# Performance work log

Hardware: AMD Instinct MI355X
Metric: run time of the kernel (lower is better)

Reference implementation:

```python
import jax, jax.numpy as jnp
import numpy as np

N_NODES = 50000


def _glorot(key, fan_in, fan_out):
    limit = float(np.sqrt(6.0 / (fan_in + fan_out)))
    return jax.random.uniform(key, (fan_in, fan_out), jnp.float32, -limit, limit)


def setup_inputs() -> dict:
    key = jax.random.key(0)
    k_x, k_src, k_dst, k1, k2, k3 = jax.random.split(key, 6)
    x = jax.random.normal(k_x, (N_NODES, 128), dtype=jnp.float32)
    src = jax.random.randint(k_src, (800000,), 0, N_NODES)
    dst = jax.random.randint(k_dst, (800000,), 0, N_NODES)
    edge_index = jnp.stack([src, dst]).astype(jnp.int64)  # [2, E]
    W1 = _glorot(k1, 128, 96)
    W2 = _glorot(k2, 96, 96)
    W3 = _glorot(k3, 96, 40)
    b1 = jnp.zeros((96,), jnp.float32)
    b2 = jnp.zeros((96,), jnp.float32)
    b3 = jnp.zeros((40,), jnp.float32)
    return {"x": x, "W1": W1, "b1": b1, "W2": W2, "b2": b2,
            "W3": W3, "b3": b3, "edge_index": edge_index}


def _aggregate(x, src, dst):
    # sparse adj SpMM with 'add' reduce: out[dst] += x[src]
    return jax.ops.segment_sum(x[src], dst, num_segments=N_NODES)


def reference(x, W1, b1, W2, b2, W3, b3, edge_index):
    src, dst = edge_index[0], edge_index[1]
    # layer 1: aggregate -> linear -> relu (dropout identity in eval)
    h = jax.nn.relu(_aggregate(x, src, dst) @ W1 + b1)
    # layer 2
    h = jax.nn.relu(_aggregate(h, src, dst) @ W2 + b2)
    # layer 3 + log_softmax
    logits = _aggregate(h, src, dst) @ W3 + b3
    return jax.nn.log_softmax(logits, axis=-1)
```

## Files before the change

### kernel.cpp

```cpp
#include <hip/hip_runtime.h>
#include <math.h>

typedef __attribute__((ext_vector_type(8))) short bf16x8;
typedef __attribute__((ext_vector_type(4))) float f32x4;

__device__ __forceinline__ unsigned short f2bf(float f) {
  unsigned u = __float_as_uint(f);
  u += 0x7fffu + ((u >> 16) & 1u);
  return (unsigned short)(u >> 16);
}
__device__ __forceinline__ float bflo(unsigned u) { return __uint_as_float(u << 16); }
__device__ __forceinline__ float bfhi(unsigned u) { return __uint_as_float(u & 0xffff0000u); }


constexpr int CB = 64;

__global__ __launch_bounds__(256) void count_pack_gemm1(
    const int* __restrict__ dst, int* __restrict__ partial, int E,
    const float* __restrict__ W1, const float* __restrict__ W2, const float* __restrict__ W3,
    unsigned short* __restrict__ Wp2, unsigned short* __restrict__ Wp3,
    const float* __restrict__ x, unsigned short* __restrict__ Tb, int N) {
  int tid = threadIdx.x;
  if (blockIdx.x < CB) {
    __shared__ int bkt[256];
    bkt[tid] = 0;
    __syncthreads();
    int E4 = E >> 2;
    const int4* d4 = (const int4*)dst;
    for (int i = blockIdx.x * 256 + tid; i < E4; i += CB * 256) {
      int4 d = d4[i];
      atomicAdd(&bkt[d.x >> 8], 1);
      atomicAdd(&bkt[d.y >> 8], 1);
      atomicAdd(&bkt[d.z >> 8], 1);
      atomicAdd(&bkt[d.w >> 8], 1);
    }
    if (blockIdx.x == 0 && tid < (E & 3)) atomicAdd(&bkt[dst[E4 * 4 + tid] >> 8], 1);
    __syncthreads();
    partial[blockIdx.x * 256 + tid] = bkt[tid];
    return;
  }
  if (blockIdx.x < CB + 7) {
    int gid = (blockIdx.x - CB) * 256 + tid;
    const float* W;
    unsigned short* Wp;
    int t, NCTT, M, MV;
    if (gid < 1152) {
      W = W2; Wp = Wp2; t = gid; NCTT = 6; M = 96; MV = 96;
    } else if (gid < 1728) {
      W = W3; Wp = Wp3; t = gid - 1152; NCTT = 3; M = 40; MV = 40;
    } else {
      return;
    }
    int lane = t & 63;
    int frag = t >> 6;
    int s = frag / NCTT;
    int ct = frag - s * NCTT;
    int colv = ct * 16 + (lane & 15);
    int k0 = s * 32 + (lane >> 4) * 8;
    union { unsigned short s[8]; uint4 u; } pk;
#pragma unroll
    for (int j = 0; j < 8; ++j) {
      float v = (colv < MV) ? W[(k0 + j) * M + colv] : 0.f;
      pk.s[j] = f2bf(v);
    }
    ((uint4*)Wp)[t] = pk.u;
    return;
  }
  int bgx = blockIdx.x - CB - 7;
  int wid = tid >> 6;
  int lane = tid & 63;
  int rt = bgx * 4 + wid;
  if (rt * 16 >= N) return;
  int quad = lane >> 4;
  int lm = lane & 15;
  bf16x8 bfrag[4][6];
#pragma unroll
  for (int s = 0; s < 4; ++s)
#pragma unroll
    for (int c = 0; c < 6; ++c) {
      union { unsigned short s[8]; bf16x8 v; } bu;
      int k0 = s * 32 + quad * 8;
      int colv = c * 16 + lm;
#pragma unroll
      for (int j = 0; j < 8; ++j) bu.s[j] = f2bf(W1[(k0 + j) * 96 + colv]);
      bfrag[s][c] = bu.v;
    }
  f32x4 acc[6];
#pragma unroll
  for (int c = 0; c < 6; ++c) acc[c] = (f32x4){0.f, 0.f, 0.f, 0.f};
  int row = rt * 16 + lm;
  if (row >= N) row = N - 1;
#pragma unroll
  for (int s = 0; s < 4; ++s) {
    int k0 = s * 32 + quad * 8;
    const float* Af = x + (size_t)row * 128 + k0;
    float4 x0 = *(const float4*)(Af);
    float4 x1 = *(const float4*)(Af + 4);
    union { unsigned short s[8]; bf16x8 v; } au;
    au.s[0] = f2bf(x0.x); au.s[1] = f2bf(x0.y); au.s[2] = f2bf(x0.z); au.s[3] = f2bf(x0.w);
    au.s[4] = f2bf(x1.x); au.s[5] = f2bf(x1.y); au.s[6] = f2bf(x1.z); au.s[7] = f2bf(x1.w);
#pragma unroll
    for (int c = 0; c < 6; ++c)
      acc[c] = __builtin_amdgcn_mfma_f32_16x16x32_bf16(au.v, bfrag[s][c], acc[c], 0, 0, 0);
  }
#pragma unroll
  for (int c = 0; c < 6; ++c) {
    int colv = c * 16 + lm;
#pragma unroll
    for (int r = 0; r < 4; ++r) {
      int orow = rt * 16 + quad * 4 + r;
      if (orow < N) Tb[(size_t)orow * 96 + colv] = f2bf(acc[c][r]);
    }
  }
}

__global__ __launch_bounds__(256) void scan_kernel(const int* __restrict__ partial,
                                                   int* __restrict__ gstart,
                                                   int* __restrict__ gcur,
                                                   int* __restrict__ row_ptr,
                                                   int NB, int N, int E) {
  int tid = threadIdx.x;
  int s = 0;
#pragma unroll 8
  for (int i = 0; i < CB; ++i) s += partial[i * 256 + tid];
  __shared__ int sm[256];
  sm[tid] = s;
  __syncthreads();
  for (int off = 1; off < 256; off <<= 1) {
    int u = (tid >= off) ? sm[tid - off] : 0;
    __syncthreads();
    sm[tid] += u;
    __syncthreads();
  }
  int excl = sm[tid] - s;
  if (tid < NB) { gstart[tid] = excl; gcur[tid] = excl; }
  if (tid == NB - 1) gstart[NB] = sm[tid];
  if (tid == 0) row_ptr[N] = E;
}

__global__ __launch_bounds__(256) void bin_edges(const int* __restrict__ src,
                                                 const int* __restrict__ dst,
                                                 int* __restrict__ gcur,
                                                 int* __restrict__ packed, int E, int NB) {
  __shared__ int lcnt[256];
  __shared__ int gbase[256];
  int tid = threadIdx.x;
  lcnt[tid] = 0;
  __syncthreads();
  int idx = blockIdx.x * 256 + tid;
  int E4 = E >> 2;
  int sv[4], dv[4], lv[4];
  int cnt = 0;
  if (idx < E4) {
    int4 s4 = ((const int4*)src)[idx];
    int4 d4 = ((const int4*)dst)[idx];
    sv[0] = s4.x; sv[1] = s4.y; sv[2] = s4.z; sv[3] = s4.w;
    dv[0] = d4.x; dv[1] = d4.y; dv[2] = d4.z; dv[3] = d4.w;
    cnt = 4;
  } else if (idx == E4 && (E & 3)) {
    int tl = E & 3;
    for (int i = 0; i < tl; ++i) { sv[i] = src[E4 * 4 + i]; dv[i] = dst[E4 * 4 + i]; }
    cnt = tl;
  }
  for (int i = 0; i < cnt; ++i) lv[i] = atomicAdd(&lcnt[dv[i] >> 8], 1);
  __syncthreads();
  if (tid < NB) gbase[tid] = atomicAdd(&gcur[tid], lcnt[tid]);
  __syncthreads();
  for (int i = 0; i < cnt; ++i) {
    int b = dv[i] >> 8;
    packed[gbase[b] + lv[i]] = ((dv[i] & 255) << 16) | (sv[i] & 0xffff);
  }
}

__global__ __launch_bounds__(256) void build_local_csr(const int* __restrict__ packed,
                                                       const int* __restrict__ gstart,
                                                       int* __restrict__ row_ptr,
                                                       int* __restrict__ col, int N) {
  __shared__ int cnt[256];
  __shared__ int sm[256];
  int b = blockIdx.x, tid = threadIdx.x;
  int gs = gstart[b], ge = gstart[b + 1];
  int me = ge - gs;
  int node0 = b << 8;
  int RL = N - node0;
  if (RL > 256) RL = 256;
  cnt[tid] = 0;
  __syncthreads();
  for (int i = tid; i < me; i += 256) atomicAdd(&cnt[packed[gs + i] >> 16], 1);
  __syncthreads();
  int v = cnt[tid];
  sm[tid] = v;
  __syncthreads();
  for (int off = 1; off < 256; off <<= 1) {
    int u = (tid >= off) ? sm[tid - off] : 0;
    __syncthreads();
    sm[tid] += u;
    __syncthreads();
  }
  int excl = gs + sm[tid] - v;
  __syncthreads();
  cnt[tid] = excl;
  if (tid < RL) row_ptr[node0 + tid] = excl;
  __syncthreads();
  for (int i = tid; i < me; i += 256) {
    int pk = packed[gs + i];
    int p = atomicAdd(&cnt[pk >> 16], 1);
    col[p] = pk & 0xffff;
  }
}


template <int NCT, int MOUT, int MVALID>
__global__ __launch_bounds__(256) void fused_agg_gemm(const unsigned short* __restrict__ tin,
                                                      const int* __restrict__ row_ptr,
                                                      const int* __restrict__ col,
                                                      const float* __restrict__ bias,
                                                      const unsigned short* __restrict__ Wp,
                                                      unsigned short* __restrict__ outp, int N) {
  constexpr int LST = 104;
  constexpr int CAP = 2048;
  __shared__ unsigned short sH[64 * LST];
  __shared__ int scol[CAP];
  __shared__ int srp[65];
  int tid = threadIdx.x;
  int node0 = blockIdx.x * 64;
  int nloc = N - node0;
  if (nloc > 64) nloc = 64;
  if (tid <= nloc) srp[tid] = row_ptr[node0 + tid];
  __syncthreads();
  int gs = srp[0];
  int me = srp[nloc] - gs;
  for (int i = tid; i < me && i < CAP; i += 256) scol[i] = col[gs + i];
  __syncthreads();

#pragma unroll
  for (int it = 0; it < 3; ++it) {
    int u = tid + it * 256;
    int nl = u / 12;
    int c = u - nl * 12;
    if (nl < nloc) {
      int beg = srp[nl] - gs;
      int end = srp[nl + 1] - gs;
      const unsigned short* tc = tin + 8 * c;
      float a0 = 0.f, a1 = 0.f, a2 = 0.f, a3 = 0.f, a4 = 0.f, a5 = 0.f, a6 = 0.f, a7 = 0.f;
      int e = beg;
      for (; e + 1 < end; e += 2) {
        int s0 = (e < CAP) ? scol[e] : col[gs + e];
        int s1 = (e + 1 < CAP) ? scol[e + 1] : col[gs + e + 1];
        uint4 u4 = *(const uint4*)(tc + (size_t)s0 * 96);
        uint4 w4 = *(const uint4*)(tc + (size_t)s1 * 96);
        a0 += bflo(u4.x); a1 += bfhi(u4.x);
        a2 += bflo(u4.y); a3 += bfhi(u4.y);
        a4 += bflo(u4.z); a5 += bfhi(u4.z);
        a6 += bflo(u4.w); a7 += bfhi(u4.w);
        a0 += bflo(w4.x); a1 += bfhi(w4.x);
        a2 += bflo(w4.y); a3 += bfhi(w4.y);
        a4 += bflo(w4.z); a5 += bfhi(w4.z);
        a6 += bflo(w4.w); a7 += bfhi(w4.w);
      }
      if (e < end) {
        int s0 = (e < CAP) ? scol[e] : col[gs + e];
        uint4 u4 = *(const uint4*)(tc + (size_t)s0 * 96);
        a0 += bflo(u4.x); a1 += bfhi(u4.x);
        a2 += bflo(u4.y); a3 += bfhi(u4.y);
        a4 += bflo(u4.z); a5 += bfhi(u4.z);
        a6 += bflo(u4.w); a7 += bfhi(u4.w);
      }
      const float* b = bias + 8 * c;
      union { unsigned short s[8]; uint4 u; } pk;
      pk.s[0] = f2bf(fmaxf(a0 + b[0], 0.f));
      pk.s[1] = f2bf(fmaxf(a1 + b[1], 0.f));
      pk.s[2] = f2bf(fmaxf(a2 + b[2], 0.f));
      pk.s[3] = f2bf(fmaxf(a3 + b[3], 0.f));
      pk.s[4] = f2bf(fmaxf(a4 + b[4], 0.f));
      pk.s[5] = f2bf(fmaxf(a5 + b[5], 0.f));
      pk.s[6] = f2bf(fmaxf(a6 + b[6], 0.f));
      pk.s[7] = f2bf(fmaxf(a7 + b[7], 0.f));
      *(uint4*)&sH[nl * LST + c * 8] = pk.u;
    }
  }
  __syncthreads();

  int wid = tid >> 6;
  int lane = tid & 63;
  int rt16 = wid * 16;
  if (node0 + rt16 >= N) return;
  int quad = lane >> 4;
  int lm = lane & 15;
  union BU { uint4 u; bf16x8 v; };
  bf16x8 bfrag[3][NCT];
  const uint4* wp4 = (const uint4*)Wp;
#pragma unroll
  for (int s = 0; s < 3; ++s)
#pragma unroll
    for (int c = 0; c < NCT; ++c) {
      BU bu;
      bu.u = wp4[(s * NCT + c) * 64 + lane];
      bfrag[s][c] = bu.v;
    }
  f32x4 acc[NCT];
#pragma unroll
  for (int c = 0; c < NCT; ++c) acc[c] = (f32x4){0.f, 0.f, 0.f, 0.f};
#pragma unroll
  for (int s = 0; s < 3; ++s) {
    BU au;
    au.u = *(const uint4*)&sH[(rt16 + lm) * LST + s * 32 + quad * 8];
#pragma unroll
    for (int c = 0; c < NCT; ++c)
      acc[c] = __builtin_amdgcn_mfma_f32_16x16x32_bf16(au.v, bfrag[s][c], acc[c], 0, 0, 0);
  }
#pragma unroll
  for (int c = 0; c < NCT; ++c) {
    int colv = c * 16 + lm;
    if (colv >= MVALID) continue;
#pragma unroll
    for (int r = 0; r < 4; ++r) {
      int orow = node0 + rt16 + quad * 4 + r;
      if (orow < N) outp[(size_t)orow * MOUT + colv] = f2bf(acc[c][r]);
    }
  }
}

__global__ __launch_bounds__(256) void agg_lsm_bf16(const unsigned short* __restrict__ t,
                                                    const int* __restrict__ row_ptr,
                                                    const int* __restrict__ col,
                                                    const float* __restrict__ bias,
                                                    float* __restrict__ out, int N) {
  constexpr int CAPL = 1024;
  __shared__ int scol[CAPL];
  __shared__ int srp[17];
  int tid = threadIdx.x;
  int node0 = blockIdx.x * 16;
  int nloc = N - node0;
  if (nloc > 16) nloc = 16;
  if (tid <= nloc) srp[tid] = row_ptr[node0 + tid];
  __syncthreads();
  int gs = srp[0];
  int me = srp[nloc] - gs;
  for (int i = tid; i < me && i < CAPL; i += 256) scol[i] = col[gs + i];
  __syncthreads();

  int nl = tid >> 4;
  int c = tid & 15;
  bool act = (c < 10) && (nl < nloc);
  int ceff = (c < 10) ? c : 0;
  const unsigned short* tc = t + 4 * ceff;
  float v0 = 0.f, v1 = 0.f, v2 = 0.f, v3 = 0.f;
  if (act) {
    int beg = srp[nl] - gs;
    int end = srp[nl + 1] - gs;
    int e = beg;
    for (; e + 1 < end; e += 2) {
      int s0 = (e < CAPL) ? scol[e] : col[gs + e];
      int s1 = (e + 1 < CAPL) ? scol[e + 1] : col[gs + e + 1];
      uint2 u = *(const uint2*)(tc + (size_t)s0 * 40);
      uint2 w = *(const uint2*)(tc + (size_t)s1 * 40);
      v0 += bflo(u.x); v1 += bfhi(u.x);
      v2 += bflo(u.y); v3 += bfhi(u.y);
      v0 += bflo(w.x); v1 += bfhi(w.x);
      v2 += bflo(w.y); v3 += bfhi(w.y);
    }
    if (e < end) {
      int s0 = (e < CAPL) ? scol[e] : col[gs + e];
      uint2 u = *(const uint2*)(tc + (size_t)s0 * 40);
      v0 += bflo(u.x); v1 += bfhi(u.x);
      v2 += bflo(u.y); v3 += bfhi(u.y);
    }
  }
  const float* bb = bias + 4 * ceff;
  v0 += bb[0]; v1 += bb[1]; v2 += bb[2]; v3 += bb[3];
  float m = act ? fmaxf(fmaxf(v0, v1), fmaxf(v2, v3)) : -__builtin_inff();
#pragma unroll
  for (int off = 8; off; off >>= 1) m = fmaxf(m, __shfl_xor(m, off, 64));
  float ex = act ? (__expf(v0 - m) + __expf(v1 - m) + __expf(v2 - m) + __expf(v3 - m)) : 0.f;
#pragma unroll
  for (int off = 8; off; off >>= 1) ex += __shfl_xor(ex, off, 64);
  if (act) {
    int node = node0 + nl;
    float l = m + __logf(ex);
    float* o = out + (size_t)node * 40 + 4 * c;
    o[0] = v0 - l; o[1] = v1 - l; o[2] = v2 - l; o[3] = v3 - l;
  }
}


extern "C" void kernel_launch(void* const* d_in, const int* in_sizes, int n_in,
                              void* d_out, int out_size, void* d_ws, size_t ws_size,
                              hipStream_t stream) {
  const float* x  = (const float*)d_in[0];
  const float* W1 = (const float*)d_in[1];
  const float* b1 = (const float*)d_in[2];
  const float* W2 = (const float*)d_in[3];
  const float* b2 = (const float*)d_in[4];
  const float* W3 = (const float*)d_in[5];
  const float* b3 = (const float*)d_in[6];
  const int* edge = (const int*)d_in[7];

  int N = in_sizes[0] / 128;
  int E = in_sizes[7] / 2;
  const int* srcp = edge;
  const int* dstp = edge + E;

  char* p = (char*)d_ws;
  auto alloc = [&](size_t bytes) {
    char* r = p;
    p += (bytes + 255) & ~size_t(255);
    return r;
  };
  int NB = (N + 255) >> 8;
  int* partial = (int*)alloc((size_t)CB * 256 * 4);
  int* gstart  = (int*)alloc((size_t)(NB + 1) * 4);
  int* gcur    = (int*)alloc((size_t)NB * 4);
  int* row_ptr = (int*)alloc((size_t)(N + 1) * 4);
  int* packed  = (int*)alloc((size_t)E * 4);
  int* col     = (int*)alloc((size_t)E * 4);
  unsigned short* Wp2 = (unsigned short*)alloc(1152 * 8 * 2);
  unsigned short* Wp3 = (unsigned short*)alloc(576 * 8 * 2);
  unsigned short* Tb  = (unsigned short*)alloc((size_t)N * 96 * 2);
  unsigned short* T2b = (unsigned short*)alloc((size_t)N * 96 * 2);
  unsigned short* T3b = (unsigned short*)alloc((size_t)N * 40 * 2);

  int E4 = E >> 2;
  int nbin = (E4 + ((E & 3) ? 1 : 0) + 255) / 256;
  int GB = ((N + 15) / 16 + 3) / 4;
  int FB = (N + 63) / 64;

  count_pack_gemm1<<<CB + 7 + GB, 256, 0, stream>>>(dstp, partial, E, W1, W2, W3,
                                                    Wp2, Wp3, x, Tb, N);
  scan_kernel<<<1, 256, 0, stream>>>(partial, gstart, gcur, row_ptr, NB, N, E);
  bin_edges<<<nbin, 256, 0, stream>>>(srcp, dstp, gcur, packed, E, NB);
  build_local_csr<<<NB, 256, 0, stream>>>(packed, gstart, row_ptr, col, N);
  fused_agg_gemm<6, 96, 96><<<FB, 256, 0, stream>>>(Tb, row_ptr, col, b1, Wp2, T2b, N);
  fused_agg_gemm<3, 40, 40><<<FB, 256, 0, stream>>>(T2b, row_ptr, col, b2, Wp3, T3b, N);
  agg_lsm_bf16<<<(N + 15) / 16, 256, 0, stream>>>(T3b, row_ptr, col, b3, (float*)d_out, N);
}
```

Measured before the change: 209.8 us.

## Move layer-1 GEMM into binning kernel, prepack W1, unroll gathers by four

W1 is now pre-packed to bf16 MFMA fragments in the count/pack kernel. The layer-1 x@W1 GEMM moves from the counting kernel into the edge-binning kernel, so it overlaps with binning, and it reads the packed W1 instead of converting W1 in every wave. The neighbour-gather loops in the aggregation kernels are unrolled from two to four loads in flight. fused_agg_gemm gets a min-waves occupancy hint and loads B fragments inside the MFMA loop instead of keeping them all in registers. These changes target per-wave conversion cost, register pressure and gather latency, at the risk of a longer critical path through bin_gemm1 and extra global loads of weight fragments.

```diff
diff --git a/kernel.cpp b/kernel.cpp
--- a/kernel.cpp
+++ b/kernel.cpp
@@ -15,11 +15,14 @@
 
 constexpr int CB = 64;
 
-__global__ __launch_bounds__(256) void count_pack_gemm1(
-    const int* __restrict__ dst, int* __restrict__ partial, int E,
-    const float* __restrict__ W1, const float* __restrict__ W2, const float* __restrict__ W3,
-    unsigned short* __restrict__ Wp2, unsigned short* __restrict__ Wp3,
-    const float* __restrict__ x, unsigned short* __restrict__ Tb, int N) {
+__global__ __launch_bounds__(256) void count_pack(const int* __restrict__ dst,
+                                                  int* __restrict__ partial, int E,
+                                                  const float* __restrict__ W1,
+                                                  const float* __restrict__ W2,
+                                                  const float* __restrict__ W3,
+                                                  unsigned short* __restrict__ Wp1,
+                                                  unsigned short* __restrict__ Wp2,
+                                                  unsigned short* __restrict__ Wp3) {
   int tid = threadIdx.x;
   if (blockIdx.x < CB) {
     __shared__ int bkt[256];
@@ -39,79 +42,32 @@
     partial[blockIdx.x * 256 + tid] = bkt[tid];
     return;
   }
-  if (blockIdx.x < CB + 7) {
-    int gid = (blockIdx.x - CB) * 256 + tid;
-    const float* W;
-    unsigned short* Wp;
-    int t, NCTT, M, MV;
-    if (gid < 1152) {
-      W = W2; Wp = Wp2; t = gid; NCTT = 6; M = 96; MV = 96;
-    } else if (gid < 1728) {
-      W = W3; Wp = Wp3; t = gid - 1152; NCTT = 3; M = 40; MV = 40;
-    } else {
-      return;
-    }
-    int lane = t & 63;
-    int frag = t >> 6;
-    int s = frag / NCTT;
-    int ct = frag - s * NCTT;
-    int colv = ct * 16 + (lane & 15);
-    int k0 = s * 32 + (lane >> 4) * 8;
-    union { unsigned short s[8]; uint4 u; } pk;
-#pragma unroll
-    for (int j = 0; j < 8; ++j) {
-      float v = (colv < MV) ? W[(k0 + j) * M + colv] : 0.f;
-      pk.s[j] = f2bf(v);
-    }
-    ((uint4*)Wp)[t] = pk.u;
+  int gid = (blockIdx.x - CB) * 256 + tid;
+  const float* W;
+  unsigned short* Wp;
+  int t, NCTT, M, MV;
+  if (gid < 1536) {
+    W = W1; Wp = Wp1; t = gid; NCTT = 6; M = 96; MV = 96;
+  } else if (gid < 2688) {
+    W = W2; Wp = Wp2; t = gid - 1536; NCTT = 6; M = 96; MV = 96;
+  } else if (gid < 3264) {
+    W = W3; Wp = Wp3; t = gid - 2688; NCTT = 3; M = 40; MV = 40;
+  } else {
     return;
   }
-  int bgx = blockIdx.x - CB - 7;
-  int wid = tid >> 6;
-  int lane = tid & 63;
-  int rt = bgx * 4 + wid;
-  if (rt * 16 >= N) return;
-  int quad = lane >> 4;
-  int lm = lane & 15;
-  bf16x8 bfrag[4][6];
-#pragma unroll
-  for (int s = 0; s < 4; ++s)
-#pragma unroll
-    for (int c = 0; c < 6; ++c) {
-      union { unsigned short s[8]; bf16x8 v; } bu;
-      int k0 = s * 32 + quad * 8;
-      int colv = c * 16 + lm;
-#pragma unroll
-      for (int j = 0; j < 8; ++j) bu.s[j] = f2bf(W1[(k0 + j) * 96 + colv]);
-      bfrag[s][c] = bu.v;
-    }
-  f32x4 acc[6];
-#pragma unroll
-  for (int c = 0; c < 6; ++c) acc[c] = (f32x4){0.f, 0.f, 0.f, 0.f};
-  int row = rt * 16 + lm;
-  if (row >= N) row = N - 1;
-#pragma unroll
-  for (int s = 0; s < 4; ++s) {
-    int k0 = s * 32 + quad * 8;
-    const float* Af = x + (size_t)row * 128 + k0;
-    float4 x0 = *(const float4*)(Af);
-    float4 x1 = *(const float4*)(Af + 4);
-    union { unsigned short s[8]; bf16x8 v; } au;
-    au.s[0] = f2bf(x0.x); au.s[1] = f2bf(x0.y); au.s[2] = f2bf(x0.z); au.s[3] = f2bf(x0.w);
-    au.s[4] = f2bf(x1.x); au.s[5] = f2bf(x1.y); au.s[6] = f2bf(x1.z); au.s[7] = f2bf(x1.w);
-#pragma unroll
-    for (int c = 0; c < 6; ++c)
-      acc[c] = __builtin_amdgcn_mfma_f32_16x16x32_bf16(au.v, bfrag[s][c], acc[c], 0, 0, 0);
-  }
-#pragma unroll
-  for (int c = 0; c < 6; ++c) {
-    int colv = c * 16 + lm;
-#pragma unroll
-    for (int r = 0; r < 4; ++r) {
-      int orow = rt * 16 + quad * 4 + r;
-      if (orow < N) Tb[(size_t)orow * 96 + colv] = f2bf(acc[c][r]);
-    }
-  }
+  int lane = t & 63;
+  int frag = t >> 6;
+  int s = frag / NCTT;
+  int ct = frag - s * NCTT;
+  int colv = ct * 16 + (lane & 15);
+  int k0 = s * 32 + (lane >> 4) * 8;
+  union { unsigned short s[8]; uint4 u; } pk;
+#pragma unroll
+  for (int j = 0; j < 8; ++j) {
+    float v = (colv < MV) ? W[(k0 + j) * M + colv] : 0.f;
+    pk.s[j] = f2bf(v);
+  }
+  ((uint4*)Wp)[t] = pk.u;
 }
 
 __global__ __launch_bounds__(256) void scan_kernel(const int* __restrict__ partial,
@@ -138,37 +94,82 @@
   if (tid == 0) row_ptr[N] = E;
 }
 
-__global__ __launch_bounds__(256) void bin_edges(const int* __restrict__ src,
+__global__ __launch_bounds__(256) void bin_gemm1(const int* __restrict__ src,
                                                  const int* __restrict__ dst,
                                                  int* __restrict__ gcur,
-                                                 int* __restrict__ packed, int E, int NB) {
-  __shared__ int lcnt[256];
-  __shared__ int gbase[256];
+                                                 int* __restrict__ packed, int E, int NB,
+                                                 int NBIN, const float* __restrict__ x,
+                                                 const unsigned short* __restrict__ Wp1,
+                                                 unsigned short* __restrict__ Tb, int N) {
   int tid = threadIdx.x;
-  lcnt[tid] = 0;
-  __syncthreads();
-  int idx = blockIdx.x * 256 + tid;
-  int E4 = E >> 2;
-  int sv[4], dv[4], lv[4];
-  int cnt = 0;
-  if (idx < E4) {
-    int4 s4 = ((const int4*)src)[idx];
-    int4 d4 = ((const int4*)dst)[idx];
-    sv[0] = s4.x; sv[1] = s4.y; sv[2] = s4.z; sv[3] = s4.w;
-    dv[0] = d4.x; dv[1] = d4.y; dv[2] = d4.z; dv[3] = d4.w;
-    cnt = 4;
-  } else if (idx == E4 && (E & 3)) {
-    int tl = E & 3;
-    for (int i = 0; i < tl; ++i) { sv[i] = src[E4 * 4 + i]; dv[i] = dst[E4 * 4 + i]; }
-    cnt = tl;
-  }
-  for (int i = 0; i < cnt; ++i) lv[i] = atomicAdd(&lcnt[dv[i] >> 8], 1);
-  __syncthreads();
-  if (tid < NB) gbase[tid] = atomicAdd(&gcur[tid], lcnt[tid]);
-  __syncthreads();
-  for (int i = 0; i < cnt; ++i) {
-    int b = dv[i] >> 8;
-    packed[gbase[b] + lv[i]] = ((dv[i] & 255) << 16) | (sv[i] & 0xffff);
+  if (blockIdx.x < NBIN) {
+    __shared__ int lcnt[256];
+    __shared__ int gbase[256];
+    lcnt[tid] = 0;
+    __syncthreads();
+    int idx = blockIdx.x * 256 + tid;
+    int E4 = E >> 2;
+    int sv[4], dv[4], lv[4];
+    int cnt = 0;
+    if (idx < E4) {
+      int4 s4 = ((const int4*)src)[idx];
+      int4 d4 = ((const int4*)dst)[idx];
+      sv[0] = s4.x; sv[1] = s4.y; sv[2] = s4.z; sv[3] = s4.w;
+      dv[0] = d4.x; dv[1] = d4.y; dv[2] = d4.z; dv[3] = d4.w;
+      cnt = 4;
+    } else if (idx == E4 && (E & 3)) {
+      int tl = E & 3;
+      for (int i = 0; i < tl; ++i) { sv[i] = src[E4 * 4 + i]; dv[i] = dst[E4 * 4 + i]; }
+      cnt = tl;
+    }
+    for (int i = 0; i < cnt; ++i) lv[i] = atomicAdd(&lcnt[dv[i] >> 8], 1);
+    __syncthreads();
+    if (tid < NB) gbase[tid] = atomicAdd(&gcur[tid], lcnt[tid]);
+    __syncthreads();
+    for (int i = 0; i < cnt; ++i) {
+      int b = dv[i] >> 8;
+      packed[gbase[b] + lv[i]] = ((dv[i] & 255) << 16) | (sv[i] & 0xffff);
+    }
+    return;
+  }
+  int bx = blockIdx.x - NBIN;
+  int wid = tid >> 6;
+  int lane = tid & 63;
+  int rt = bx * 4 + wid;
+  if (rt * 16 >= N) return;
+  int quad = lane >> 4;
+  int lm = lane & 15;
+  union BU { uint4 u; bf16x8 v; };
+  f32x4 acc[6];
+#pragma unroll
+  for (int c = 0; c < 6; ++c) acc[c] = (f32x4){0.f, 0.f, 0.f, 0.f};
+  int row = rt * 16 + lm;
+  if (row >= N) row = N - 1;
+  const uint4* wp4 = (const uint4*)Wp1;
+#pragma unroll
+  for (int s = 0; s < 4; ++s) {
+    int k0 = s * 32 + quad * 8;
+    const float* Af = x + (size_t)row * 128 + k0;
+    float4 x0 = *(const float4*)(Af);
+    float4 x1 = *(const float4*)(Af + 4);
+    union { unsigned short s[8]; bf16x8 v; } au;
+    au.s[0] = f2bf(x0.x); au.s[1] = f2bf(x0.y); au.s[2] = f2bf(x0.z); au.s[3] = f2bf(x0.w);
+    au.s[4] = f2bf(x1.x); au.s[5] = f2bf(x1.y); au.s[6] = f2bf(x1.z); au.s[7] = f2bf(x1.w);
+#pragma unroll
+    for (int c = 0; c < 6; ++c) {
+      BU bu;
+      bu.u = wp4[(s * 6 + c) * 64 + lane];
+      acc[c] = __builtin_amdgcn_mfma_f32_16x16x32_bf16(au.v, bu.v, acc[c], 0, 0, 0);
+    }
+  }
+#pragma unroll
+  for (int c = 0; c < 6; ++c) {
+    int colv = c * 16 + lm;
+#pragma unroll
+    for (int r = 0; r < 4; ++r) {
+      int orow = rt * 16 + quad * 4 + r;
+      if (orow < N) Tb[(size_t)orow * 96 + colv] = f2bf(acc[c][r]);
+    }
   }
 }
 
@@ -211,12 +212,10 @@
 
 
 template <int NCT, int MOUT, int MVALID>
-__global__ __launch_bounds__(256) void fused_agg_gemm(const unsigned short* __restrict__ tin,
-                                                      const int* __restrict__ row_ptr,
-                                                      const int* __restrict__ col,
-                                                      const float* __restrict__ bias,
-                                                      const unsigned short* __restrict__ Wp,
-                                                      unsigned short* __restrict__ outp, int N) {
+__global__ __launch_bounds__(256, 6) void fused_agg_gemm(
+    const unsigned short* __restrict__ tin, const int* __restrict__ row_ptr,
+    const int* __restrict__ col, const float* __restrict__ bias,
+    const unsigned short* __restrict__ Wp, unsigned short* __restrict__ outp, int N) {
   constexpr int LST = 104;
   constexpr int CAP = 2048;
   __shared__ unsigned short sH[64 * LST];
@@ -244,27 +243,29 @@
       const unsigned short* tc = tin + 8 * c;
       float a0 = 0.f, a1 = 0.f, a2 = 0.f, a3 = 0.f, a4 = 0.f, a5 = 0.f, a6 = 0.f, a7 = 0.f;
       int e = beg;
-      for (; e + 1 < end; e += 2) {
+      for (; e + 3 < end; e += 4) {
         int s0 = (e < CAP) ? scol[e] : col[gs + e];
         int s1 = (e + 1 < CAP) ? scol[e + 1] : col[gs + e + 1];
-        uint4 u4 = *(const uint4*)(tc + (size_t)s0 * 96);
-        uint4 w4 = *(const uint4*)(tc + (size_t)s1 * 96);
-        a0 += bflo(u4.x); a1 += bfhi(u4.x);
-        a2 += bflo(u4.y); a3 += bfhi(u4.y);
-        a4 += bflo(u4.z); a5 += bfhi(u4.z);
-        a6 += bflo(u4.w); a7 += bfhi(u4.w);
-        a0 += bflo(w4.x); a1 += bfhi(w4.x);
-        a2 += bflo(w4.y); a3 += bfhi(w4.y);
-        a4 += bflo(w4.z); a5 += bfhi(w4.z);
-        a6 += bflo(w4.w); a7 += bfhi(w4.w);
+        int s2 = (e + 2 < CAP) ? scol[e + 2] : col[gs + e + 2];
+        int s3 = (e + 3 < CAP) ? scol[e + 3] : col[gs + e + 3];
+        uint4 u0 = *(const uint4*)(tc + (size_t)s0 * 96);
+        uint4 u1 = *(const uint4*)(tc + (size_t)s1 * 96);
+        uint4 u2 = *(const uint4*)(tc + (size_t)s2 * 96);
+        uint4 u3 = *(const uint4*)(tc + (size_t)s3 * 96);
+        a0 += bflo(u0.x); a1 += bfhi(u0.x); a2 += bflo(u0.y); a3 += bfhi(u0.y);
+        a4 += bflo(u0.z); a5 += bfhi(u0.z); a6 += bflo(u0.w); a7 += bfhi(u0.w);
+        a0 += bflo(u1.x); a1 += bfhi(u1.x); a2 += bflo(u1.y); a3 += bfhi(u1.y);
+        a4 += bflo(u1.z); a5 += bfhi(u1.z); a6 += bflo(u1.w); a7 += bfhi(u1.w);
+        a0 += bflo(u2.x); a1 += bfhi(u2.x); a2 += bflo(u2.y); a3 += bfhi(u2.y);
+        a4 += bflo(u2.z); a5 += bfhi(u2.z); a6 += bflo(u2.w); a7 += bfhi(u2.w);
+        a0 += bflo(u3.x); a1 += bfhi(u3.x); a2 += bflo(u3.y); a3 += bfhi(u3.y);
+        a4 += bflo(u3.z); a5 += bfhi(u3.z); a6 += bflo(u3.w); a7 += bfhi(u3.w);
       }
-      if (e < end) {
+      for (; e < end; ++e) {
         int s0 = (e < CAP) ? scol[e] : col[gs + e];
         uint4 u4 = *(const uint4*)(tc + (size_t)s0 * 96);
-        a0 += bflo(u4.x); a1 += bfhi(u4.x);
-        a2 += bflo(u4.y); a3 += bfhi(u4.y);
-        a4 += bflo(u4.z); a5 += bfhi(u4.z);
-        a6 += bflo(u4.w); a7 += bfhi(u4.w);
+        a0 += bflo(u4.x); a1 += bfhi(u4.x); a2 += bflo(u4.y); a3 += bfhi(u4.y);
+        a4 += bflo(u4.z); a5 += bfhi(u4.z); a6 += bflo(u4.w); a7 += bfhi(u4.w);
       }
       const float* b = bias + 8 * c;
       union { unsigned short s[8]; uint4 u; } pk;
@@ -288,26 +289,20 @@
   int quad = lane >> 4;
   int lm = lane & 15;
   union BU { uint4 u; bf16x8 v; };
-  bf16x8 bfrag[3][NCT];
+  f32x4 acc[NCT];
+#pragma unroll
+  for (int c = 0; c < NCT; ++c) acc[c] = (f32x4){0.f, 0.f, 0.f, 0.f};
   const uint4* wp4 = (const uint4*)Wp;
 #pragma unroll
-  for (int s = 0; s < 3; ++s)
+  for (int s = 0; s < 3; ++s) {
+    BU au;
+    au.u = *(const uint4*)&sH[(rt16 + lm) * LST + s * 32 + quad * 8];
 #pragma unroll
     for (int c = 0; c < NCT; ++c) {
       BU bu;
       bu.u = wp4[(s * NCT + c) * 64 + lane];
-      bfrag[s][c] = bu.v;
-    }
-  f32x4 acc[NCT];
-#pragma unroll
-  for (int c = 0; c < NCT; ++c) acc[c] = (f32x4){0.f, 0.f, 0.f, 0.f};
-#pragma unroll
-  for (int s = 0; s < 3; ++s) {
-    BU au;
-    au.u = *(const uint4*)&sH[(rt16 + lm) * LST + s * 32 + quad * 8];
-#pragma unroll
-    for (int c = 0; c < NCT; ++c)
-      acc[c] = __builtin_amdgcn_mfma_f32_16x16x32_bf16(au.v, bfrag[s][c], acc[c], 0, 0, 0);
+      acc[c] = __builtin_amdgcn_mfma_f32_16x16x32_bf16(au.v, bu.v, acc[c], 0, 0, 0);
+    }
   }
 #pragma unroll
   for (int c = 0; c < NCT; ++c) {
@@ -350,21 +345,24 @@
     int beg = srp[nl] - gs;
     int end = srp[nl + 1] - gs;
     int e = beg;
-    for (; e + 1 < end; e += 2) {
+    for (; e + 3 < end; e += 4) {
       int s0 = (e < CAPL) ? scol[e] : col[gs + e];
       int s1 = (e + 1 < CAPL) ? scol[e + 1] : col[gs + e + 1];
+      int s2 = (e + 2 < CAPL) ? scol[e + 2] : col[gs + e + 2];
+      int s3 = (e + 3 < CAPL) ? scol[e + 3] : col[gs + e + 3];
       uint2 u = *(const uint2*)(tc + (size_t)s0 * 40);
       uint2 w = *(const uint2*)(tc + (size_t)s1 * 40);
-      v0 += bflo(u.x); v1 += bfhi(u.x);
-      v2 += bflo(u.y); v3 += bfhi(u.y);
-      v0 += bflo(w.x); v1 += bfhi(w.x);
-      v2 += bflo(w.y); v3 += bfhi(w.y);
-    }
-    if (e < end) {
+      uint2 y = *(const uint2*)(tc + (size_t)s2 * 40);
+      uint2 z = *(const uint2*)(tc + (size_t)s3 * 40);
+      v0 += bflo(u.x); v1 += bfhi(u.x); v2 += bflo(u.y); v3 += bfhi(u.y);
+      v0 += bflo(w.x); v1 += bfhi(w.x); v2 += bflo(w.y); v3 += bfhi(w.y);
+      v0 += bflo(y.x); v1 += bfhi(y.x); v2 += bflo(y.y); v3 += bfhi(y.y);
+      v0 += bflo(z.x); v1 += bfhi(z.x); v2 += bflo(z.y); v3 += bfhi(z.y);
+    }
+    for (; e < end; ++e) {
       int s0 = (e < CAPL) ? scol[e] : col[gs + e];
       uint2 u = *(const uint2*)(tc + (size_t)s0 * 40);
-      v0 += bflo(u.x); v1 += bfhi(u.x);
-      v2 += bflo(u.y); v3 += bfhi(u.y);
+      v0 += bflo(u.x); v1 += bfhi(u.x); v2 += bflo(u.y); v3 += bfhi(u.y);
     }
   }
   const float* bb = bias + 4 * ceff;
@@ -414,6 +412,7 @@
   int* row_ptr = (int*)alloc((size_t)(N + 1) * 4);
   int* packed  = (int*)alloc((size_t)E * 4);
   int* col     = (int*)alloc((size_t)E * 4);
+  unsigned short* Wp1 = (unsigned short*)alloc(1536 * 8 * 2);
   unsigned short* Wp2 = (unsigned short*)alloc(1152 * 8 * 2);
   unsigned short* Wp3 = (unsigned short*)alloc(576 * 8 * 2);
   unsigned short* Tb  = (unsigned short*)alloc((size_t)N * 96 * 2);
@@ -425,10 +424,10 @@
   int GB = ((N + 15) / 16 + 3) / 4;
   int FB = (N + 63) / 64;
 
-  count_pack_gemm1<<<CB + 7 + GB, 256, 0, stream>>>(dstp, partial, E, W1, W2, W3,
-                                                    Wp2, Wp3, x, Tb, N);
+  count_pack<<<CB + 13, 256, 0, stream>>>(dstp, partial, E, W1, W2, W3, Wp1, Wp2, Wp3);
   scan_kernel<<<1, 256, 0, stream>>>(partial, gstart, gcur, row_ptr, NB, N, E);
-  bin_edges<<<nbin, 256, 0, stream>>>(srcp, dstp, gcur, packed, E, NB);
+  bin_gemm1<<<nbin + GB, 256, 0, stream>>>(srcp, dstp, gcur, packed, E, NB, nbin,
+                                           x, Wp1, Tb, N);
   build_local_csr<<<NB, 256, 0, stream>>>(packed, gstart, row_ptr, col, N);
   fused_agg_gemm<6, 96, 96><<<FB, 256, 0, stream>>>(Tb, row_ptr, col, b1, Wp2, T2b, N);
   fused_agg_gemm<3, 40, 40><<<FB, 256, 0, stream>>>(T2b, row_ptr, col, b2, Wp3, T3b, N);
```

After: 203.1 us. 1.03x faster.
